# Optimization experiments

Hardware: AMD Instinct MI355X
Metric: run time of the kernel (lower is better)

## Reference

```python
import jax, jax.numpy as jnp
import numpy as np

E = 8      # num_experts
K = 2      # top-k
HID = 2048 # per-expert hidden dim


def setup_inputs() -> dict:
    key = jax.random.key(0)
    ks = jax.random.split(key, 7)
    D = 1024
    x = jax.random.normal(ks[0], (4, 2048, D), dtype=jnp.float32)
    Wr = jax.random.normal(ks[1], (D, E), dtype=jnp.float32) * 0.02
    br = jnp.zeros((E,), jnp.float32)
    W1 = jax.random.normal(ks[2], (E, D, 2 * HID), dtype=jnp.float32) * 0.02
    b1 = jnp.zeros((E, 2 * HID), jnp.float32)
    W2 = jax.random.normal(ks[3], (E, HID, D), dtype=jnp.float32) * 0.02
    b2 = jnp.zeros((E, D), jnp.float32)
    return {"x": x, "Wr": Wr, "br": br, "W1": W1, "b1": b1, "W2": W2, "b2": b2}


def reference(x, Wr, br, W1, b1, W2, b2):
    B, T, D = x.shape
    xf = x.reshape(-1, D)                               # [N, D]

    # --- router ---
    logits = xf @ Wr + br                               # [N, E]
    probs = jax.nn.softmax(logits, axis=-1)
    topk_val, topk_idx = jax.lax.top_k(logits, K)       # [N, K]
    scores = jax.nn.softmax(topk_val, axis=-1)          # [N, K]

    # --- load-balancing aux loss ---
    one_hot = jax.nn.one_hot(topk_idx, E, dtype=jnp.float32)   # [N, K, E]
    f = one_hot.sum(axis=1).mean(axis=0)                # [E] fraction routed
    p = probs.mean(axis=0)                              # [E] mean prob
    aux_loss = E * jnp.sum(jax.lax.stop_gradient(f) * p)

    # --- every expert over all tokens (faithful to naive module) ---
    h = jnp.einsum('nd,edh->enh', xf, W1) + b1[:, None, :]     # [E, N, 2H]
    a, b = h[..., :HID], h[..., HID:]
    g = jax.nn.silu(a) * b                              # swiglu, [E, N, H]
    oe = jnp.einsum('enh,ehd->end', g, W2) + b2[:, None, :]    # [E, N, D]

    # --- combine: gather each token's top-k expert outputs, weight, sum ---
    oe = oe.transpose(1, 0, 2)                          # [N, E, D]
    sel = jnp.take_along_axis(oe, topk_idx[:, :, None], axis=1)  # [N, K, D]
    out = (sel * scores[:, :, None]).sum(axis=1)        # [N, D]

    return out.reshape(B, T, D), aux_loss
```

## Files before the change

kernel.cpp:

```cpp
#include <hip/hip_runtime.h>
#include <hip/hip_bf16.h>
#include <math.h>

typedef __attribute__((ext_vector_type(8))) __bf16 bh8;
typedef __attribute__((ext_vector_type(4))) float  f4;

#define NTOK   8192
#define DIM    1024
#define HIDK   2048

#define OFF_CNT    0
#define OFF_PSUM   64
#define OFF_OFFS   128
#define OFF_ROWS   512
#define OFF_GATES  (512+262144)
#define OFF_XBF    524800
#define OFF_G      (524800+16777216)
#define OFF_W1S    (OFF_G + 68157440)
#define OFF_W2S    (OFF_W1S + 67108864)

__device__ __forceinline__ unsigned short f2bf(float x){
    union { float f; unsigned u; } v; v.f = x;
    unsigned r = v.u + 0x7FFFu + ((v.u >> 16) & 1u);
    return (unsigned short)(r >> 16);
}
__device__ __forceinline__ unsigned pk2(float a, float b){
    return (unsigned)f2bf(a) | ((unsigned)f2bf(b) << 16);
}
__device__ __forceinline__ void gload_lds16(const void* g, void* l){
    __builtin_amdgcn_global_load_lds((const __attribute__((address_space(1))) void*)g,
                                     (__attribute__((address_space(3))) void*)l, 16, 0, 0);
}

__global__ void convert_x(const float* __restrict__ x, short* __restrict__ xbf){
    size_t i = ((size_t)blockIdx.x * 256 + threadIdx.x) * 8;
    const float4* s = (const float4*)(x + i);
    float4 a = s[0], b = s[1];
    uint4 u;
    u.x = pk2(a.x, a.y); u.y = pk2(a.z, a.w);
    u.z = pk2(b.x, b.y); u.w = pk2(b.z, b.w);
    *(uint4*)(xbf + i) = u;
}

__global__ void prep_w(const float* __restrict__ W, short* __restrict__ Ws,
                       int Kdim, int Ndim){
    int kb = blockIdx.x, nb = blockIdx.y, e = blockIdx.z;
    int KB = Kdim >> 5, NB = Ndim >> 7;
    __shared__ float tile[32 * 132];
    int t = threadIdx.x;
    const float* src = W + ((size_t)(e * Kdim + kb * 32)) * Ndim + (size_t)nb * 128;
    #pragma unroll
    for (int l = 0; l < 4; l++){
        int flat = (l * 256 + t) * 4;
        int k = flat >> 7, n = flat & 127;
        float4 v = *(const float4*)(src + (size_t)k * Ndim + n);
        float* d = &tile[k * 132 + n];
        d[0] = v.x; d[1] = v.y; d[2] = v.z; d[3] = v.w;
    }
    __syncthreads();
    short* dst = Ws + (((size_t)(e * NB + nb)) * KB + kb) * 4096;
    uint out[8];
    #pragma unroll
    for (int sl = 0; sl < 2; sl++){
        int s = t * 2 + sl;
        int nl = s >> 2, pos = s & 3;
        int c = pos ^ (nl & 3) ^ ((nl >> 2) & 3);
        #pragma unroll
        for (int jj = 0; jj < 4; jj++){
            float a = tile[(c * 8 + jj * 2) * 132 + nl];
            float b = tile[(c * 8 + jj * 2 + 1) * 132 + nl];
            out[sl * 4 + jj] = pk2(a, b);
        }
    }
    *(uint4*)(dst + t * 16)     = *(uint4*)&out[0];
    *(uint4*)(dst + t * 16 + 8) = *(uint4*)&out[4];
}

__global__ void router(const float* __restrict__ x, const float* __restrict__ Wr,
                       const float* __restrict__ br,
                       int* cnt, float* psum, int* rows, float* gates){
    __shared__ float pP[8];
    __shared__ int   tE[32][2];
    __shared__ float tS[32][2];
    __shared__ int   lcnt[8], lpos[64], lexp[64], gbase[8];
    int t = threadIdx.x, lane = t & 63, w = t >> 6;
    if (t < 8){ pP[t] = 0.f; lcnt[t] = 0; }
    __syncthreads();
    int n0 = blockIdx.x * 32 + w * 8;
    for (int tk = 0; tk < 8; tk++){
        int n = n0 + tk;
        float acc[8] = {0,0,0,0,0,0,0,0};
        const float* xr = x + (size_t)n * DIM;
        for (int d = lane; d < DIM; d += 64){
            float xv = xr[d];
            const float* wrow = Wr + d * 8;
            #pragma unroll
            for (int e = 0; e < 8; e++) acc[e] += xv * wrow[e];
        }
        #pragma unroll
        for (int e = 0; e < 8; e++){
            float v = acc[e];
            v += __shfl_xor(v, 32); v += __shfl_xor(v, 16); v += __shfl_xor(v, 8);
            v += __shfl_xor(v, 4);  v += __shfl_xor(v, 2);  v += __shfl_xor(v, 1);
            acc[e] = v;
        }
        if (lane == 0){
            float l[8], ex[8], m = -1e30f;
            #pragma unroll
            for (int e = 0; e < 8; e++){ l[e] = acc[e] + br[e]; m = fmaxf(m, l[e]); }
            float s = 0.f;
            #pragma unroll
            for (int e = 0; e < 8; e++){ ex[e] = expf(l[e] - m); s += ex[e]; }
            float inv = 1.f / s;
            #pragma unroll
            for (int e = 0; e < 8; e++) atomicAdd(&pP[e], ex[e] * inv);
            int i0 = 0; float v0 = l[0];
            #pragma unroll
            for (int e = 1; e < 8; e++) if (l[e] > v0){ v0 = l[e]; i0 = e; }
            int i1 = -1; float v1 = -1e30f;
            #pragma unroll
            for (int e = 0; e < 8; e++) if (e != i0 && l[e] > v1){ v1 = l[e]; i1 = e; }
            float s0 = 1.f / (1.f + expf(v1 - v0));
            int ti = w * 8 + tk;
            tE[ti][0] = i0; tE[ti][1] = i1;
            tS[ti][0] = s0; tS[ti][1] = 1.f - s0;
        }
    }
    __syncthreads();
    if (t < 64){
        int e = tE[t >> 1][t & 1];
        lexp[t] = e;
        lpos[t] = atomicAdd(&lcnt[e], 1);
    }
    __syncthreads();
    if (t < 8){
        gbase[t] = atomicAdd(&cnt[t], lcnt[t]);
        atomicAdd(&psum[t], pP[t]);
    }
    __syncthreads();
    if (t < 64){
        int e = lexp[t];
        int p = gbase[e] + lpos[t];
        int n = blockIdx.x * 32 + (t >> 1);
        rows[e * NTOK + p]  = n;
        gates[e * NTOK + p] = tS[t >> 1][t & 1];
    }
}

__global__ void finalize_aux(const int* cnt, const float* psum, int* offs, float* out_aux){
    if (threadIdx.x == 0){
        int off = 0; float aux = 0.f;
        for (int e = 0; e < 8; e++){
            offs[e] = off; off += cnt[e];
            aux += ((float)cnt[e] * (1.f/8192.f)) * (psum[e] * (1.f/8192.f));
        }
        out_aux[0] = 8.f * aux;
    }
}

__global__ __launch_bounds__(256) void gemm1(
    const short* __restrict__ xbf, const short* __restrict__ W1s,
    const float* __restrict__ b1, const int* __restrict__ cnt,
    const int* __restrict__ offs, const int* __restrict__ rows,
    short* __restrict__ g)
{
    int e = blockIdx.z;
    int Me = cnt[e];
    int mbase = blockIdx.y << 7;
    if (mbase >= Me) return;
    int xB = blockIdx.x;
    __shared__ short As [2][128 * 32];
    __shared__ short Bsa[2][64 * 32];
    __shared__ short Bsb[2][64 * 32];

    int t = threadIdx.x, lane = t & 63, w = t >> 6;
    int wr = w & 1, wc = w >> 1;
    int m = lane & 15, q = lane >> 4;
    int sw8 = (q ^ (m & 3) ^ ((m >> 2) & 3)) << 3;

    const int* rowsE = rows + (e << 13) + mbase;
    int r = t >> 2, pos = t & 3;
    int ca = pos ^ (r & 3) ^ ((r >> 2) & 3);
    int tok0 = (mbase + r      < Me) ? rowsE[r]      : 0;
    int tok1 = (mbase + r + 64 < Me) ? rowsE[r + 64] : 0;
    const short* ga0 = xbf + ((size_t)tok0 << 10) + (ca << 3);
    const short* ga1 = xbf + ((size_t)tok1 << 10) + (ca << 3);
    int ha = xB & 1, nb128 = xB >> 1;
    const short* gb0 = W1s + ((size_t)((e * 32 + nb128)      * 32)) * 4096 + (ha * 256 + t) * 8;
    const short* gb1 = W1s + ((size_t)((e * 32 + 16 + nb128) * 32)) * 4096 + (ha * 256 + t) * 8;

    f4 acc_a[4][2], acc_b[4][2];
    f4 zz = {0.f,0.f,0.f,0.f};
    #pragma unroll
    for (int i = 0; i < 4; i++)
        #pragma unroll
        for (int j = 0; j < 2; j++){ acc_a[i][j] = zz; acc_b[i][j] = zz; }

    gload_lds16(ga0, &As [0][w * 512]);
    gload_lds16(ga1, &As [0][2048 + w * 512]);
    gload_lds16(gb0, &Bsa[0][w * 512]);
    gload_lds16(gb1, &Bsb[0][w * 512]);
    ga0 += 32; ga1 += 32; gb0 += 4096; gb1 += 4096;
    __syncthreads();

    int cur = 0;
    #pragma unroll 2
    for (int k0 = 0; k0 < DIM; k0 += 32){
        if (k0 + 32 < DIM){
            int nb = cur ^ 1;
            gload_lds16(ga0, &As [nb][w * 512]);
            gload_lds16(ga1, &As [nb][2048 + w * 512]);
            gload_lds16(gb0, &Bsa[nb][w * 512]);
            gload_lds16(gb1, &Bsb[nb][w * 512]);
            ga0 += 32; ga1 += 32; gb0 += 4096; gb1 += 4096;
        }
        bh8 av[4], ba[2], bb[2];
        #pragma unroll
        for (int i = 0; i < 4; i++)
            av[i] = *(const bh8*)&As[cur][(wr*64 + i*16 + m) * 32 + sw8];
        #pragma unroll
        for (int j = 0; j < 2; j++){
            int nn = ((wc << 5) + j*16 + m) * 32 + sw8;
            ba[j] = *(const bh8*)&Bsa[cur][nn];
            bb[j] = *(const bh8*)&Bsb[cur][nn];
        }
        #pragma unroll
        for (int i = 0; i < 4; i++)
            #pragma unroll
            for (int j = 0; j < 2; j++){
                acc_a[i][j] = __builtin_amdgcn_mfma_f32_16x16x32_bf16(av[i], ba[j], acc_a[i][j], 0, 0, 0);
                acc_b[i][j] = __builtin_amdgcn_mfma_f32_16x16x32_bf16(av[i], bb[j], acc_b[i][j], 0, 0, 0);
            }
        __syncthreads();
        cur ^= 1;
    }
    int c0 = xB << 6;
    const float* b1e = b1 + (e << 12);
    int colb = (wc << 5) + m;
    float vba[2], vbb[2];
    #pragma unroll
    for (int j = 0; j < 2; j++){
        vba[j] = b1e[c0 + colb + j*16];
        vbb[j] = b1e[HIDK + c0 + colb + j*16];
    }
    int rb = wr * 64 + (q << 2);
    short* gE = g + ((size_t)(offs[e] + mbase)) * HIDK;
    #pragma unroll
    for (int i = 0; i < 4; i++)
        #pragma unroll
        for (int reg = 0; reg < 4; reg++){
            int mr = rb + i*16 + reg;
            if (mbase + mr < Me){
                short* grow = gE + (size_t)mr * HIDK + c0 + colb;
                #pragma unroll
                for (int j = 0; j < 2; j++){
                    float va = acc_a[i][j][reg] + vba[j];
                    float vb = acc_b[i][j][reg] + vbb[j];
                    grow[j*16] = (short)f2bf(va / (1.f + __expf(-va)) * vb);
                }
            }
        }
}

__global__ __launch_bounds__(256) void gemm2(
    const short* __restrict__ g, const short* __restrict__ W2s,
    const float* __restrict__ b2, const int* __restrict__ cnt,
    const int* __restrict__ offs, const int* __restrict__ rows,
    const float* __restrict__ gates, float* __restrict__ out)
{
    int e = blockIdx.z;
    int Me = cnt[e];
    int mbase = blockIdx.y << 7;
    if (mbase >= Me) return;
    int db = blockIdx.x;
    __shared__ short As[2][128 * 32];
    __shared__ short Bs[2][128 * 32];

    int t = threadIdx.x, lane = t & 63, w = t >> 6;
    int wr = w & 1, wc = w >> 1;
    int m = lane & 15, q = lane >> 4;
    int sw8 = (q ^ (m & 3) ^ ((m >> 2) & 3)) << 3;

    int gbaseR = offs[e] + mbase;
    int r = t >> 2;
    int ca = (t & 3) ^ (r & 3) ^ ((r >> 2) & 3);
    const short* ga0 = g + ((size_t)(gbaseR + r))      * HIDK + (ca << 3);
    const short* ga1 = g + ((size_t)(gbaseR + r + 64)) * HIDK + (ca << 3);
    const short* gb0 = W2s + ((size_t)((e * 8 + db) * 64)) * 4096 + t * 8;
    const short* gb1 = gb0 + 2048;

    f4 acc[4][4];
    f4 zz = {0.f,0.f,0.f,0.f};
    #pragma unroll
    for (int i = 0; i < 4; i++)
        #pragma unroll
        for (int j = 0; j < 4; j++) acc[i][j] = zz;

    gload_lds16(ga0, &As[0][w * 512]);
    gload_lds16(ga1, &As[0][2048 + w * 512]);
    gload_lds16(gb0, &Bs[0][w * 512]);
    gload_lds16(gb1, &Bs[0][2048 + w * 512]);
    ga0 += 32; ga1 += 32; gb0 += 4096; gb1 += 4096;
    __syncthreads();

    int cur = 0;
    #pragma unroll 2
    for (int k0 = 0; k0 < HIDK; k0 += 32){
        if (k0 + 32 < HIDK){
            int nb = cur ^ 1;
            gload_lds16(ga0, &As[nb][w * 512]);
            gload_lds16(ga1, &As[nb][2048 + w * 512]);
            gload_lds16(gb0, &Bs[nb][w * 512]);
            gload_lds16(gb1, &Bs[nb][2048 + w * 512]);
            ga0 += 32; ga1 += 32; gb0 += 4096; gb1 += 4096;
        }
        bh8 av[4], bv[4];
        #pragma unroll
        for (int i = 0; i < 4; i++)
            av[i] = *(const bh8*)&As[cur][(wr*64 + i*16 + m) * 32 + sw8];
        #pragma unroll
        for (int j = 0; j < 4; j++)
            bv[j] = *(const bh8*)&Bs[cur][(wc*64 + j*16 + m) * 32 + sw8];
        #pragma unroll
        for (int i = 0; i < 4; i++)
            #pragma unroll
            for (int j = 0; j < 4; j++)
                acc[i][j] = __builtin_amdgcn_mfma_f32_16x16x32_bf16(av[i], bv[j], acc[i][j], 0, 0, 0);
        __syncthreads();
        cur ^= 1;
    }
    int d0 = db << 7;
    const float* b2e = b2 + (e << 10);
    int colb = wc * 64 + m;
    float vb2[4];
    #pragma unroll
    for (int j = 0; j < 4; j++) vb2[j] = b2e[d0 + colb + j*16];
    const int* rowsE = rows + (e << 13) + mbase;
    const float* gatesE = gates + (e << 13) + mbase;
    int rb = wr * 64 + (q << 2);
    #pragma unroll
    for (int i = 0; i < 4; i++)
        #pragma unroll
        for (int reg = 0; reg < 4; reg++){
            int mr = rb + i*16 + reg;
            if (mbase + mr < Me){
                int token = rowsE[mr];
                float gate = gatesE[mr];
                float* orow = out + ((size_t)token << 10) + d0 + colb;
                #pragma unroll
                for (int j = 0; j < 4; j++)
                    unsafeAtomicAdd(&orow[j*16], gate * (acc[i][j][reg] + vb2[j]));
            }
        }
}

extern "C" void kernel_launch(void* const* d_in, const int* in_sizes, int n_in,
                              void* d_out, int out_size, void* d_ws, size_t ws_size,
                              hipStream_t stream) {
    const float* x  = (const float*)d_in[0];
    const float* Wr = (const float*)d_in[1];
    const float* br = (const float*)d_in[2];
    const float* W1 = (const float*)d_in[3];
    const float* b1 = (const float*)d_in[4];
    const float* W2 = (const float*)d_in[5];
    const float* b2 = (const float*)d_in[6];
    float* out = (float*)d_out;

    char* ws = (char*)d_ws;
    int*   cnt   = (int*)(ws + OFF_CNT);
    float* psum  = (float*)(ws + OFF_PSUM);
    int*   offs  = (int*)(ws + OFF_OFFS);
    int*   rows  = (int*)(ws + OFF_ROWS);
    float* gates = (float*)(ws + OFF_GATES);
    short* xbf   = (short*)(ws + OFF_XBF);
    short* g     = (short*)(ws + OFF_G);
    short* W1s   = (short*)(ws + OFF_W1S);
    short* W2s   = (short*)(ws + OFF_W2S);

    hipMemsetAsync(ws, 0, 192, stream);
    hipMemsetAsync(d_out, 0, (size_t)NTOK * DIM * 4, stream);

    prep_w<<<dim3(32, 32, 8), 256, 0, stream>>>(W1, W1s, 1024, 4096);
    prep_w<<<dim3(64, 8, 8),  256, 0, stream>>>(W2, W2s, 2048, 1024);
    convert_x<<<4096, 256, 0, stream>>>(x, xbf);
    router<<<256, 256, 0, stream>>>(x, Wr, br, cnt, psum, rows, gates);
    finalize_aux<<<1, 64, 0, stream>>>(cnt, psum, offs, out + (size_t)NTOK * DIM);
    gemm1<<<dim3(32, 64, 8), 256, 0, stream>>>(xbf, W1s, b1, cnt, offs, rows, g);
    gemm2<<<dim3(8, 64, 8),  256, 0, stream>>>(g, W2s, b2, cnt, offs, rows, gates, out);
}
```

Measured before the change: 778.9 us.

## Replace double-buffered prefetch with single-stage K=64 load-then-compute loop in expert GEMMs

Both expert GEMM kernels (gate/up and down projection) drop the double-buffered prefetch pipeline. Each iteration now loads two 32-wide K slices into both LDS buffers, synchronizes, and computes both slices. This halves the number of loop iterations and barrier pairs per K step and issues more loads at once, but global loads no longer overlap with MFMA work inside a block. It relies on other resident blocks to hide memory latency.

```diff
diff --git a/kernel.cpp b/kernel.cpp
--- a/kernel.cpp
+++ b/kernel.cpp
@@ -196,43 +196,38 @@
         #pragma unroll
         for (int j = 0; j < 2; j++){ acc_a[i][j] = zz; acc_b[i][j] = zz; }
 
-    gload_lds16(ga0, &As [0][w * 512]);
-    gload_lds16(ga1, &As [0][2048 + w * 512]);
-    gload_lds16(gb0, &Bsa[0][w * 512]);
-    gload_lds16(gb1, &Bsb[0][w * 512]);
-    ga0 += 32; ga1 += 32; gb0 += 4096; gb1 += 4096;
-    __syncthreads();
-
-    int cur = 0;
-    #pragma unroll 2
-    for (int k0 = 0; k0 < DIM; k0 += 32){
-        if (k0 + 32 < DIM){
-            int nb = cur ^ 1;
-            gload_lds16(ga0, &As [nb][w * 512]);
-            gload_lds16(ga1, &As [nb][2048 + w * 512]);
-            gload_lds16(gb0, &Bsa[nb][w * 512]);
-            gload_lds16(gb1, &Bsb[nb][w * 512]);
-            ga0 += 32; ga1 += 32; gb0 += 4096; gb1 += 4096;
-        }
-        bh8 av[4], ba[2], bb[2];
-        #pragma unroll
-        for (int i = 0; i < 4; i++)
-            av[i] = *(const bh8*)&As[cur][(wr*64 + i*16 + m) * 32 + sw8];
-        #pragma unroll
-        for (int j = 0; j < 2; j++){
-            int nn = ((wc << 5) + j*16 + m) * 32 + sw8;
-            ba[j] = *(const bh8*)&Bsa[cur][nn];
-            bb[j] = *(const bh8*)&Bsb[cur][nn];
-        }
-        #pragma unroll
-        for (int i = 0; i < 4; i++)
+    for (int k0 = 0; k0 < DIM; k0 += 64){
+        __syncthreads();
+        gload_lds16(ga0,        &As [0][w * 512]);
+        gload_lds16(ga0 + 32,   &As [1][w * 512]);
+        gload_lds16(ga1,        &As [0][2048 + w * 512]);
+        gload_lds16(ga1 + 32,   &As [1][2048 + w * 512]);
+        gload_lds16(gb0,        &Bsa[0][w * 512]);
+        gload_lds16(gb0 + 4096, &Bsa[1][w * 512]);
+        gload_lds16(gb1,        &Bsb[0][w * 512]);
+        gload_lds16(gb1 + 4096, &Bsb[1][w * 512]);
+        ga0 += 64; ga1 += 64; gb0 += 8192; gb1 += 8192;
+        __syncthreads();
+        #pragma unroll
+        for (int c2 = 0; c2 < 2; c2++){
+            bh8 av[4], ba[2], bb[2];
+            #pragma unroll
+            for (int i = 0; i < 4; i++)
+                av[i] = *(const bh8*)&As[c2][(wr*64 + i*16 + m) * 32 + sw8];
             #pragma unroll
             for (int j = 0; j < 2; j++){
-                acc_a[i][j] = __builtin_amdgcn_mfma_f32_16x16x32_bf16(av[i], ba[j], acc_a[i][j], 0, 0, 0);
-                acc_b[i][j] = __builtin_amdgcn_mfma_f32_16x16x32_bf16(av[i], bb[j], acc_b[i][j], 0, 0, 0);
+                int nn = ((wc << 5) + j*16 + m) * 32 + sw8;
+                ba[j] = *(const bh8*)&Bsa[c2][nn];
+                bb[j] = *(const bh8*)&Bsb[c2][nn];
             }
-        __syncthreads();
-        cur ^= 1;
+            #pragma unroll
+            for (int i = 0; i < 4; i++)
+                #pragma unroll
+                for (int j = 0; j < 2; j++){
+                    acc_a[i][j] = __builtin_amdgcn_mfma_f32_16x16x32_bf16(av[i], ba[j], acc_a[i][j], 0, 0, 0);
+                    acc_b[i][j] = __builtin_amdgcn_mfma_f32_16x16x32_bf16(av[i], bb[j], acc_b[i][j], 0, 0, 0);
+                }
+        }
     }
     int c0 = xB << 6;
     const float* b1e = b1 + (e << 12);
@@ -296,38 +291,33 @@
         #pragma unroll
         for (int j = 0; j < 4; j++) acc[i][j] = zz;
 
-    gload_lds16(ga0, &As[0][w * 512]);
-    gload_lds16(ga1, &As[0][2048 + w * 512]);
-    gload_lds16(gb0, &Bs[0][w * 512]);
-    gload_lds16(gb1, &Bs[0][2048 + w * 512]);
-    ga0 += 32; ga1 += 32; gb0 += 4096; gb1 += 4096;
-    __syncthreads();
-
-    int cur = 0;
-    #pragma unroll 2
-    for (int k0 = 0; k0 < HIDK; k0 += 32){
-        if (k0 + 32 < HIDK){
-            int nb = cur ^ 1;
-            gload_lds16(ga0, &As[nb][w * 512]);
-            gload_lds16(ga1, &As[nb][2048 + w * 512]);
-            gload_lds16(gb0, &Bs[nb][w * 512]);
-            gload_lds16(gb1, &Bs[nb][2048 + w * 512]);
-            ga0 += 32; ga1 += 32; gb0 += 4096; gb1 += 4096;
-        }
-        bh8 av[4], bv[4];
-        #pragma unroll
-        for (int i = 0; i < 4; i++)
-            av[i] = *(const bh8*)&As[cur][(wr*64 + i*16 + m) * 32 + sw8];
-        #pragma unroll
-        for (int j = 0; j < 4; j++)
-            bv[j] = *(const bh8*)&Bs[cur][(wc*64 + j*16 + m) * 32 + sw8];
-        #pragma unroll
-        for (int i = 0; i < 4; i++)
+    for (int k0 = 0; k0 < HIDK; k0 += 64){
+        __syncthreads();
+        gload_lds16(ga0,        &As[0][w * 512]);
+        gload_lds16(ga0 + 32,   &As[1][w * 512]);
+        gload_lds16(ga1,        &As[0][2048 + w * 512]);
+        gload_lds16(ga1 + 32,   &As[1][2048 + w * 512]);
+        gload_lds16(gb0,        &Bs[0][w * 512]);
+        gload_lds16(gb0 + 4096, &Bs[1][w * 512]);
+        gload_lds16(gb1,        &Bs[0][2048 + w * 512]);
+        gload_lds16(gb1 + 4096, &Bs[1][2048 + w * 512]);
+        ga0 += 64; ga1 += 64; gb0 += 8192; gb1 += 8192;
+        __syncthreads();
+        #pragma unroll
+        for (int c2 = 0; c2 < 2; c2++){
+            bh8 av[4], bv[4];
+            #pragma unroll
+            for (int i = 0; i < 4; i++)
+                av[i] = *(const bh8*)&As[c2][(wr*64 + i*16 + m) * 32 + sw8];
             #pragma unroll
             for (int j = 0; j < 4; j++)
-                acc[i][j] = __builtin_amdgcn_mfma_f32_16x16x32_bf16(av[i], bv[j], acc[i][j], 0, 0, 0);
-        __syncthreads();
-        cur ^= 1;
+                bv[j] = *(const bh8*)&Bs[c2][(wc*64 + j*16 + m) * 32 + sw8];
+            #pragma unroll
+            for (int i = 0; i < 4; i++)
+                #pragma unroll
+                for (int j = 0; j < 4; j++)
+                    acc[i][j] = __builtin_amdgcn_mfma_f32_16x16x32_bf16(av[i], bv[j], acc[i][j], 0, 0, 0);
+        }
     }
     int d0 = db << 7;
     const float* b2e = b2 + (e << 10);
```

Measured after the change: 718.5 us. -7.7%, faster.
